# Kernel tuning notes

Hardware: AMD Instinct MI355X
Metric: run time of the kernel (lower is better)

Reference implementation:

```python
import jax, jax.numpy as jnp
import numpy as np

HEADS = 8


def setup_inputs() -> dict:
    key = jax.random.key(0)
    ks = jax.random.split(key, 6)
    B, N, D = 4, 2048, 512
    return {
        "x": jax.random.normal(ks[0], (B, N, D), dtype=jnp.float32),
        "pos": jax.random.uniform(ks[1], (B, N, 3), dtype=jnp.float32),
        "qkv_w": jax.random.normal(ks[2], (3 * D, D), dtype=jnp.float32) * 0.02,
        "qkv_b": jax.random.normal(ks[3], (3 * D,), dtype=jnp.float32) * 0.02,
        "out_w": jax.random.normal(ks[4], (D, D), dtype=jnp.float32) * 0.02,
        "out_b": jax.random.normal(ks[5], (D,), dtype=jnp.float32) * 0.02,
    }


def reference(x, pos, qkv_w, qkv_b, out_w, out_b):
    B, N, D = x.shape
    H = HEADS
    Dh = D // H
    scale = D ** (-0.5)  # NOTE: original uses full dim, not head dim

    # QKV projection -> [3, B, H, N, Dh]
    qkv = (x @ qkv_w.T + qkv_b).reshape(B, N, 3, H, Dh).transpose(2, 0, 3, 1, 4)
    q, k, v = qkv[0], qkv[1], qkv[2]

    # partial 3D RoPE on first 6 head dims (3 axis pairs)
    theta = pos * jnp.pi                    # [B, N, 3]
    sin = jnp.sin(theta)[:, None]           # [B, 1, N, 3] broadcasts over heads
    cos = jnp.cos(theta)[:, None]

    def rotate(t):
        x_rot = t[..., :6]
        x1 = x_rot[..., 0::2]               # [B, H, N, 3]
        x2 = x_rot[..., 1::2]
        return jnp.concatenate(
            [x1 * cos - x2 * sin, x1 * sin + x2 * cos, t[..., 6:]], axis=-1
        )

    q = rotate(q)
    k = rotate(k)

    attn = jax.nn.softmax(jnp.einsum("bhqd,bhkd->bhqk", q, k) * scale, axis=-1)
    out = jnp.einsum("bhqk,bhkd->bhqd", attn, v)          # [B, H, N, Dh]
    out = out.transpose(0, 2, 1, 3).reshape(B, N, D)
    return out @ out_w.T + out_b
```

## Files before the change

kernel.cpp:

```cpp
#include <hip/hip_runtime.h>
#include <stdint.h>

typedef __attribute__((ext_vector_type(4))) float f32x4;
typedef __attribute__((ext_vector_type(16))) float f32x16;
typedef __attribute__((ext_vector_type(8))) short bf16x8;
typedef __attribute__((ext_vector_type(4))) unsigned short u16x4;

__device__ __forceinline__ unsigned short f2bf(float f) {
    unsigned int u = __builtin_bit_cast(unsigned int, f);
    u += 0x7fffu + ((u >> 16) & 1u);
    return (unsigned short)(u >> 16);
}
__device__ __forceinline__ float bf2f(unsigned short s) {
    unsigned int u = ((unsigned int)s) << 16;
    return __builtin_bit_cast(float, u);
}
__device__ __forceinline__ float fexp2(float x) {
#if __has_builtin(__builtin_amdgcn_exp2f)
    return __builtin_amdgcn_exp2f(x);
#else
    return exp2f(x);
#endif
}
__device__ __forceinline__ unsigned int cvt_pk_bf16(float lo, float hi) {
    unsigned int r;
    asm("v_cvt_pk_bf16_f32 %0, %1, %2" : "=v"(r) : "v"(lo), "v"(hi));
    return r;
}

__global__ void k_cvt3(const float* __restrict__ x,
                       const float* __restrict__ w1,
                       const float* __restrict__ w2,
                       unsigned short* __restrict__ out) {
    const int C1 = 1048576;
    const int C2 = 196608;
    int i = blockIdx.x * blockDim.x + threadIdx.x;
    f32x4 v;
    if (i < C1)            v = ((const f32x4*)x)[i];
    else if (i < C1 + C2)  v = ((const f32x4*)w1)[i - C1];
    else                   v = ((const f32x4*)w2)[i - C1 - C2];
    u16x4 o;
    o.x = f2bf(v.x); o.y = f2bf(v.y); o.z = f2bf(v.z); o.w = f2bf(v.w);
    ((u16x4*)out)[i] = o;
}

__global__ __launch_bounds__(256, 3)
void k_gemm_qkv(const unsigned short* __restrict__ A,
                const unsigned short* __restrict__ Bm,
                const float* __restrict__ bias,
                const float* __restrict__ pos,
                unsigned short* __restrict__ Qb,
                unsigned short* __restrict__ Kb,
                unsigned short* __restrict__ VT) {
    const float PI = 3.14159265358979323846f;
    const float QS = 0.04419417382415922f * 1.44269504088896341f;
    const int K = 512, N = 1536;
    __shared__ unsigned short As[3][128 * 32];
    __shared__ unsigned short Bs[3][128 * 32];
    const int tid = threadIdx.x;
    const int lane = tid & 63;
    const int w = tid >> 6;
    const int wr = (w >> 1) * 64, wc = (w & 1) * 64;
    const int g = lane >> 4, fr = lane & 15;

    const int bid = blockIdx.x;
    const int xcd = bid & 7, loc = bid >> 3;
    const int rowb = xcd * 8 + (loc & 7);
    const int colb = loc >> 3;

    f32x4 acc[4][4];
#pragma unroll
    for (int i = 0; i < 4; ++i)
#pragma unroll
        for (int j = 0; j < 4; ++j) acc[i][j] = f32x4{0.f, 0.f, 0.f, 0.f};

    const int srow16 = lane >> 2;
    const int schunk = ((lane & 3) ^ (srow16 & 3)) * 8;
    const int sA = w, sB = w + 4;
    const unsigned short* Aseg0 = A + (size_t)(rowb * 128 + sA * 16 + srow16) * K + schunk;
    const unsigned short* Aseg1 = A + (size_t)(rowb * 128 + sB * 16 + srow16) * K + schunk;
    const unsigned short* Bseg0 = Bm + (size_t)(colb * 128 + sA * 16 + srow16) * K + schunk;
    const unsigned short* Bseg1 = Bm + (size_t)(colb * 128 + sB * 16 + srow16) * K + schunk;

    auto stage = [&](int bsel, int k0) {
        char* la = (char*)&As[bsel][0];
        char* lb = (char*)&Bs[bsel][0];
        __builtin_amdgcn_global_load_lds((const __attribute__((address_space(1))) void*)(Aseg0 + k0),
                                         (__attribute__((address_space(3))) void*)(la + sA * 1024), 16, 0, 0);
        __builtin_amdgcn_global_load_lds((const __attribute__((address_space(1))) void*)(Aseg1 + k0),
                                         (__attribute__((address_space(3))) void*)(la + sB * 1024), 16, 0, 0);
        __builtin_amdgcn_global_load_lds((const __attribute__((address_space(1))) void*)(Bseg0 + k0),
                                         (__attribute__((address_space(3))) void*)(lb + sA * 1024), 16, 0, 0);
        __builtin_amdgcn_global_load_lds((const __attribute__((address_space(1))) void*)(Bseg1 + k0),
                                         (__attribute__((address_space(3))) void*)(lb + sB * 1024), 16, 0, 0);
    };
    auto compute = [&](int bsel) {
        bf16x8 af[4], bfv[4];
        const int rc = (g ^ (fr & 3)) * 8;
#pragma unroll
        for (int mi = 0; mi < 4; ++mi)
            af[mi] = *(const bf16x8*)&As[bsel][(wr + mi * 16 + fr) * 32 + rc];
#pragma unroll
        for (int ni = 0; ni < 4; ++ni)
            bfv[ni] = *(const bf16x8*)&Bs[bsel][(wc + ni * 16 + fr) * 32 + rc];
        __builtin_amdgcn_s_setprio(1);
#pragma unroll
        for (int mi = 0; mi < 4; ++mi)
#pragma unroll
            for (int ni = 0; ni < 4; ++ni)
                acc[mi][ni] = __builtin_amdgcn_mfma_f32_16x16x32_bf16(af[mi], bfv[ni], acc[mi][ni], 0, 0, 0);
        __builtin_amdgcn_s_setprio(0);
    };

    const int nt = K >> 5;
    stage(0, 0);
    stage(1, 32);
    int cur = 0;
#pragma unroll 1
    for (int t = 0; t < nt; ++t) {
        if (t < nt - 1) asm volatile("s_waitcnt vmcnt(4)" ::: "memory");
        else            asm volatile("s_waitcnt vmcnt(0)" ::: "memory");
        __builtin_amdgcn_s_barrier();
        compute(cur);
        if (t + 2 < nt) {
            int nxt = cur + 2; if (nxt >= 3) nxt -= 3;
            stage(nxt, (t + 2) << 5);
        }
        cur = (cur + 1 == 3) ? 0 : cur + 1;
    }

    const int jrot = (fr < 3) ? fr : ((fr < 6) ? fr - 3 : 0);
    const int shbase = lane & 48;
#pragma unroll
    for (int mi = 0; mi < 4; ++mi) {
#pragma unroll
        for (int ni = 0; ni < 4; ++ni) {
            int row = rowb * 128 + wr + mi * 16 + g * 4;
            int col = colb * 128 + wc + ni * 16 + fr;
            float bz = bias[col];
            float v[4];
#pragma unroll
            for (int r = 0; r < 4; ++r) v[r] = acc[mi][ni][r] + bz;
            int b = row >> 11, n = row & 2047;
            if (colb < 8) {
                const int isQ = (colb < 4);
                int qcol = isQ ? col : col - 512;
                int h = qcol >> 6, dh = qcol & 63;
                if (ni == 0) {
#pragma unroll
                    for (int r = 0; r < 4; ++r) {
                        float x1 = __shfl(v[r], shbase + 2 * jrot, 64);
                        float x2 = __shfl(v[r], shbase + 2 * jrot + 1, 64);
                        if (fr < 6) {
                            float th = pos[(row + r) * 3 + jrot] * PI;
                            float sn = __sinf(th), cs = __cosf(th);
                            v[r] = (fr < 3) ? (x1 * cs - x2 * sn) : (x1 * sn + x2 * cs);
                        }
                    }
                }
                float qs = isQ ? QS : 1.f;
                unsigned short* dst = isQ ? Qb : Kb;
                size_t rb = (size_t)(b * 8 + h) * 2048 + n;
#pragma unroll
                for (int r = 0; r < 4; ++r)
                    dst[(rb + r) * 64 + dh] = f2bf(v[r] * qs);
            } else {
                int vcol = col - 1024;
                int h = vcol >> 6, dh = vcol & 63;
                int q2 = (n >> 2) & 3;
                int np = n + (q2 == 1 ? 4 : (q2 == 2 ? -4 : 0));
                u16x4 o;
#pragma unroll
                for (int r = 0; r < 4; ++r) o[r] = f2bf(v[r]);
                *(u16x4*)&VT[((size_t)(b * 8 + h) * 64 + dh) * 2048 + np] = o;
            }
        }
    }
}

__global__ __launch_bounds__(256, 3)
void k_gemm_out(const unsigned short* __restrict__ A,
                const unsigned short* __restrict__ Bm,
                const float* __restrict__ bias,
                float* __restrict__ Cout, int M, int N, int K) {
    __shared__ unsigned short As[3][128 * 32];
    __shared__ unsigned short Bs[3][128 * 32];
    const int tid = threadIdx.x;
    const int lane = tid & 63;
    const int w = tid >> 6;
    const int wr = (w >> 1) * 64, wc = (w & 1) * 64;
    const int g = lane >> 4, fr = lane & 15;

    const int bid = blockIdx.x;
    const int xcd = bid & 7, loc = bid >> 3;
    const int rowb = xcd * 8 + (loc & 7);
    const int colb = loc >> 3;

    f32x4 acc[4][4];
#pragma unroll
    for (int i = 0; i < 4; ++i)
#pragma unroll
        for (int j = 0; j < 4; ++j) acc[i][j] = f32x4{0.f, 0.f, 0.f, 0.f};

    const int srow16 = lane >> 2;
    const int schunk = ((lane & 3) ^ (srow16 & 3)) * 8;
    const int sA = w, sB = w + 4;
    const unsigned short* Aseg0 = A + (size_t)(rowb * 128 + sA * 16 + srow16) * K + schunk;
    const unsigned short* Aseg1 = A + (size_t)(rowb * 128 + sB * 16 + srow16) * K + schunk;
    const unsigned short* Bseg0 = Bm + (size_t)(colb * 128 + sA * 16 + srow16) * K + schunk;
    const unsigned short* Bseg1 = Bm + (size_t)(colb * 128 + sB * 16 + srow16) * K + schunk;

    auto stage = [&](int bsel, int k0) {
        char* la = (char*)&As[bsel][0];
        char* lb = (char*)&Bs[bsel][0];
        __builtin_amdgcn_global_load_lds((const __attribute__((address_space(1))) void*)(Aseg0 + k0),
                                         (__attribute__((address_space(3))) void*)(la + sA * 1024), 16, 0, 0);
        __builtin_amdgcn_global_load_lds((const __attribute__((address_space(1))) void*)(Aseg1 + k0),
                                         (__attribute__((address_space(3))) void*)(la + sB * 1024), 16, 0, 0);
        __builtin_amdgcn_global_load_lds((const __attribute__((address_space(1))) void*)(Bseg0 + k0),
                                         (__attribute__((address_space(3))) void*)(lb + sA * 1024), 16, 0, 0);
        __builtin_amdgcn_global_load_lds((const __attribute__((address_space(1))) void*)(Bseg1 + k0),
                                         (__attribute__((address_space(3))) void*)(lb + sB * 1024), 16, 0, 0);
    };
    auto compute = [&](int bsel) {
        bf16x8 af[4], bfv[4];
        const int rc = (g ^ (fr & 3)) * 8;
#pragma unroll
        for (int mi = 0; mi < 4; ++mi)
            af[mi] = *(const bf16x8*)&As[bsel][(wr + mi * 16 + fr) * 32 + rc];
#pragma unroll
        for (int ni = 0; ni < 4; ++ni)
            bfv[ni] = *(const bf16x8*)&Bs[bsel][(wc + ni * 16 + fr) * 32 + rc];
        __builtin_amdgcn_s_setprio(1);
#pragma unroll
        for (int mi = 0; mi < 4; ++mi)
#pragma unroll
            for (int ni = 0; ni < 4; ++ni)
                acc[mi][ni] = __builtin_amdgcn_mfma_f32_16x16x32_bf16(af[mi], bfv[ni], acc[mi][ni], 0, 0, 0);
        __builtin_amdgcn_s_setprio(0);
    };

    const int nt = K >> 5;
    stage(0, 0);
    stage(1, 32);
    int cur = 0;
#pragma unroll 1
    for (int t = 0; t < nt; ++t) {
        if (t < nt - 1) asm volatile("s_waitcnt vmcnt(4)" ::: "memory");
        else            asm volatile("s_waitcnt vmcnt(0)" ::: "memory");
        __builtin_amdgcn_s_barrier();
        compute(cur);
        if (t + 2 < nt) {
            int nxt = cur + 2; if (nxt >= 3) nxt -= 3;
            stage(nxt, (t + 2) << 5);
        }
        cur = (cur + 1 == 3) ? 0 : cur + 1;
    }

#pragma unroll
    for (int mi = 0; mi < 4; ++mi) {
#pragma unroll
        for (int ni = 0; ni < 4; ++ni) {
            int row = rowb * 128 + wr + mi * 16 + g * 4;
            int col = colb * 128 + wc + ni * 16 + fr;
            float bz = bias[col];
#pragma unroll
            for (int r = 0; r < 4; ++r)
                Cout[(size_t)(row + r) * N + col] = acc[mi][ni][r] + bz;
        }
    }
}

__global__ __launch_bounds__(512, 4)
void k_attn(const unsigned short* __restrict__ Qb,
            const unsigned short* __restrict__ Kb,
            const unsigned short* __restrict__ VT,
            unsigned short* __restrict__ Ob) {
    __shared__ unsigned short smem[2][2][2][4096];
    const int tid = threadIdx.x, lane = tid & 63, w = tid >> 6;
    const int wl = w & 3, half = w >> 2;
    const int l31 = lane & 31, hi = lane >> 5;
    const int bid = blockIdx.x;
    const int bh = (bid & 7) * 4 + ((bid >> 3) >> 4);
    const int qb = (bid >> 3) & 15;
    const int b = bh >> 3, h = bh & 7;
    const int qr0 = qb * 128 + wl * 32;
    const unsigned short* Q = Qb + (size_t)bh * 2048 * 64;
    const unsigned short* K = Kb + (size_t)bh * 2048 * 64;
    const unsigned short* V = VT + (size_t)bh * 64 * 2048;
    const int thalf = half * 16;

    const int srow8 = lane >> 3;
    const int swc = ((lane & 7) ^ srow8) << 3;
    const int sA = wl, sB = wl + 4;

    bf16x8 bq[4];
#pragma unroll
    for (int ds = 0; ds < 4; ++ds)
        bq[ds] = *(const bf16x8*)&Q[(size_t)(qr0 + l31) * 64 + ds * 16 + hi * 8];

    f32x16 oT0, oT1;
#pragma unroll
    for (int i = 0; i < 16; ++i) { oT0[i] = 0.f; oT1[i] = 0.f; }
    float lpart = 0.f;

    auto stage = [&](int bsel, int t) {
        const int kv0 = t * 64;
        const unsigned short* k0 = K + (size_t)(kv0 + sA * 8 + srow8) * 64 + swc;
        const unsigned short* k1 = K + (size_t)(kv0 + sB * 8 + srow8) * 64 + swc;
        const unsigned short* v0 = V + (size_t)(sA * 8 + srow8) * 2048 + kv0 + swc;
        const unsigned short* v1 = V + (size_t)(sB * 8 + srow8) * 2048 + kv0 + swc;
        char* dk = (char*)&smem[half][0][bsel][0];
        char* dv = (char*)&smem[half][1][bsel][0];
        __builtin_amdgcn_global_load_lds((const __attribute__((address_space(1))) void*)k0,
                                         (__attribute__((address_space(3))) void*)(dk + sA * 1024), 16, 0, 0);
        __builtin_amdgcn_global_load_lds((const __attribute__((address_space(1))) void*)k1,
                                         (__attribute__((address_space(3))) void*)(dk + sB * 1024), 16, 0, 0);
        __builtin_amdgcn_global_load_lds((const __attribute__((address_space(1))) void*)v0,
                                         (__attribute__((address_space(3))) void*)(dv + sA * 1024), 16, 0, 0);
        __builtin_amdgcn_global_load_lds((const __attribute__((address_space(1))) void*)v1,
                                         (__attribute__((address_space(3))) void*)(dv + sB * 1024), 16, 0, 0);
    };

    auto pack8 = [&](const float* p) -> bf16x8 {
        union { unsigned int u[4]; bf16x8 v; } c;
        c.u[0] = cvt_pk_bf16(p[0], p[1]);
        c.u[1] = cvt_pk_bf16(p[2], p[3]);
        c.u[2] = cvt_pk_bf16(p[4], p[5]);
        c.u[3] = cvt_pk_bf16(p[6], p[7]);
        return c.v;
    };

    auto compute = [&](int bsel) {
        const unsigned short* KsC = &smem[half][0][bsel][0];
        const unsigned short* VtC = &smem[half][1][bsel][0];
        f32x16 s0, s1;
#pragma unroll
        for (int i = 0; i < 16; ++i) { s0[i] = 0.f; s1[i] = 0.f; }
        __builtin_amdgcn_s_setprio(1);
#pragma unroll
        for (int ds = 0; ds < 4; ++ds) {
            const int c = ((((ds << 1) | hi) ^ (l31 & 7)) << 3);
            bf16x8 ka0 = *(const bf16x8*)&KsC[l31 * 64 + c];
            bf16x8 ka1 = *(const bf16x8*)&KsC[(32 + l31) * 64 + c];
            s0 = __builtin_amdgcn_mfma_f32_32x32x16_bf16(ka0, bq[ds], s0, 0, 0, 0);
            s1 = __builtin_amdgcn_mfma_f32_32x32x16_bf16(ka1, bq[ds], s1, 0, 0, 0);
        }
        __builtin_amdgcn_s_setprio(0);
        float p0[16], p1[16];
        float lsum = 0.f;
#pragma unroll
        for (int r = 0; r < 16; ++r) {
            p0[r] = fexp2(s0[r]);
            p1[r] = fexp2(s1[r]);
            lsum += p0[r] + p1[r];
        }
        lpart += lsum;
        bf16x8 pb0 = pack8(p0);
        bf16x8 pb1 = pack8(p0 + 8);
        bf16x8 pb2 = pack8(p1);
        bf16x8 pb3 = pack8(p1 + 8);
        __builtin_amdgcn_s_setprio(1);
#pragma unroll
        for (int kb = 0; kb < 4; ++kb) {
            const int c = ((((kb << 1) | hi) ^ (l31 & 7)) << 3);
            bf16x8 av0 = *(const bf16x8*)&VtC[l31 * 64 + c];
            bf16x8 av1 = *(const bf16x8*)&VtC[(32 + l31) * 64 + c];
            bf16x8 pbk = (kb == 0) ? pb0 : (kb == 1) ? pb1 : (kb == 2) ? pb2 : pb3;
            oT0 = __builtin_amdgcn_mfma_f32_32x32x16_bf16(av0, pbk, oT0, 0, 0, 0);
            oT1 = __builtin_amdgcn_mfma_f32_32x32x16_bf16(av1, pbk, oT1, 0, 0, 0);
        }
        __builtin_amdgcn_s_setprio(0);
    };

    stage(0, thalf);
    asm volatile("s_waitcnt vmcnt(0)" ::: "memory");
    __builtin_amdgcn_s_barrier();
    int cur = 0;
#pragma unroll 1
    for (int t = 0; t < 16; ++t) {
        if (t < 15) stage(cur ^ 1, thalf + t + 1);
        compute(cur);
        if (t < 15) {
            asm volatile("s_waitcnt vmcnt(0)" ::: "memory");
            __builtin_amdgcn_s_barrier();
        }
        cur ^= 1;
    }

    __syncthreads();
    float* mrg = (float*)&smem[0][0][0][0];
    float* slot = mrg + (size_t)(wl * 64 + lane) * 33;
    if (half) {
#pragma unroll
        for (int i = 0; i < 16; ++i) { slot[i] = oT0[i]; slot[16 + i] = oT1[i]; }
        slot[32] = lpart;
    }
    __syncthreads();
    if (!half) {
#pragma unroll
        for (int i = 0; i < 16; ++i) { oT0[i] += slot[i]; oT1[i] += slot[16 + i]; }
        float lf = lpart + slot[32];
        lf += __shfl_xor(lf, 32, 64);
        float il = 1.f / lf;
        size_t rowbase = (size_t)(b * 2048 + qr0 + l31) * 512 + h * 64;
#pragma unroll
        for (int grp = 0; grp < 4; ++grp) {
            u16x4 o0, o1;
#pragma unroll
            for (int i = 0; i < 4; ++i) {
                o0[i] = f2bf(oT0[grp * 4 + i] * il);
                o1[i] = f2bf(oT1[grp * 4 + i] * il);
            }
            int dv0 = grp * 8 + 4 * hi;
            *(u16x4*)&Ob[rowbase + dv0] = o0;
            *(u16x4*)&Ob[rowbase + 32 + dv0] = o1;
        }
    }
}

extern "C" void kernel_launch(void* const* d_in, const int* in_sizes, int n_in,
                              void* d_out, int out_size, void* d_ws, size_t ws_size,
                              hipStream_t stream) {
    const float* x     = (const float*)d_in[0];
    const float* pos   = (const float*)d_in[1];
    const float* qkv_w = (const float*)d_in[2];
    const float* qkv_b = (const float*)d_in[3];
    const float* out_w = (const float*)d_in[4];
    const float* out_b = (const float*)d_in[5];
    float* out = (float*)d_out;

    unsigned short* Xb   = (unsigned short*)d_ws;
    unsigned short* W1b  = Xb   + (size_t)8192 * 512;
    unsigned short* W2b  = W1b  + (size_t)1536 * 512;
    unsigned short* Qb   = W2b  + (size_t)512 * 512;
    unsigned short* Kb   = Qb   + (size_t)4194304;
    unsigned short* VTb  = Kb   + (size_t)4194304;
    unsigned short* Ob   = VTb  + (size_t)4194304;

    k_cvt3<<<5120, 256, 0, stream>>>(x, qkv_w, out_w, Xb);
    k_gemm_qkv<<<768, 256, 0, stream>>>(Xb, W1b, qkv_b, pos, Qb, Kb, VTb);
    k_attn<<<512, 512, 0, stream>>>(Qb, Kb, VTb, Ob);
    k_gemm_out<<<256, 256, 0, stream>>>(Ob, W2b, out_b, out, 8192, 512, 512);
}
```

Baseline: 85.60 us.

## Process two query sub-tiles per wave in attention to reuse K/V tiles

The attention kernel now gives each wave 64 query rows (two 32-row sub-tiles) instead of 32, doubling the query block per workgroup to 256 and halving the grid to 256 blocks. Each staged K/V tile in LDS is reused for twice as many queries, which halves global-to-LDS traffic and barrier count per query. The PV MFMAs for the first sub-tile are interleaved with the exp work of the second sub-tile so matrix and vector units can overlap. In exchange, register pressure roughly doubles (launch bounds lowered to 2 blocks/SM) and fewer blocks may underfill the 256 CUs.

```diff
diff --git a/kernel.cpp b/kernel.cpp
--- a/kernel.cpp
+++ b/kernel.cpp
@@ -54,7 +54,7 @@
                 unsigned short* __restrict__ VT) {
     const float PI = 3.14159265358979323846f;
     const float QS = 0.04419417382415922f * 1.44269504088896341f;
-    const int K = 512, N = 1536;
+    const int K = 512;
     __shared__ unsigned short As[3][128 * 32];
     __shared__ unsigned short Bs[3][128 * 32];
     const int tid = threadIdx.x;
@@ -271,7 +271,7 @@
     }
 }
 
-__global__ __launch_bounds__(512, 4)
+__global__ __launch_bounds__(512, 2)
 void k_attn(const unsigned short* __restrict__ Qb,
             const unsigned short* __restrict__ Kb,
             const unsigned short* __restrict__ VT,
@@ -281,10 +281,11 @@
     const int wl = w & 3, half = w >> 2;
     const int l31 = lane & 31, hi = lane >> 5;
     const int bid = blockIdx.x;
-    const int bh = (bid & 7) * 4 + ((bid >> 3) >> 4);
-    const int qb = (bid >> 3) & 15;
+    const int loc = bid >> 3;
+    const int bh = (bid & 7) * 4 + (loc >> 3);
+    const int qb = loc & 7;
     const int b = bh >> 3, h = bh & 7;
-    const int qr0 = qb * 128 + wl * 32;
+    const int qr0 = qb * 256 + wl * 64;
     const unsigned short* Q = Qb + (size_t)bh * 2048 * 64;
     const unsigned short* K = Kb + (size_t)bh * 2048 * 64;
     const unsigned short* V = VT + (size_t)bh * 64 * 2048;
@@ -294,15 +295,17 @@
     const int swc = ((lane & 7) ^ srow8) << 3;
     const int sA = wl, sB = wl + 4;
 
-    bf16x8 bq[4];
-#pragma unroll
-    for (int ds = 0; ds < 4; ++ds)
-        bq[ds] = *(const bf16x8*)&Q[(size_t)(qr0 + l31) * 64 + ds * 16 + hi * 8];
-
-    f32x16 oT0, oT1;
-#pragma unroll
-    for (int i = 0; i < 16; ++i) { oT0[i] = 0.f; oT1[i] = 0.f; }
-    float lpart = 0.f;
+    bf16x8 bq0[4], bq1[4];
+#pragma unroll
+    for (int ds = 0; ds < 4; ++ds) {
+        bq0[ds] = *(const bf16x8*)&Q[(size_t)(qr0 + l31) * 64 + ds * 16 + hi * 8];
+        bq1[ds] = *(const bf16x8*)&Q[(size_t)(qr0 + 32 + l31) * 64 + ds * 16 + hi * 8];
+    }
+
+    f32x16 oT00, oT01, oT10, oT11;
+#pragma unroll
+    for (int i = 0; i < 16; ++i) { oT00[i] = 0.f; oT01[i] = 0.f; oT10[i] = 0.f; oT11[i] = 0.f; }
+    float lp0 = 0.f, lp1 = 0.f;
 
     auto stage = [&](int bsel, int t) {
         const int kv0 = t * 64;
@@ -334,41 +337,75 @@
     auto compute = [&](int bsel) {
         const unsigned short* KsC = &smem[half][0][bsel][0];
         const unsigned short* VtC = &smem[half][1][bsel][0];
-        f32x16 s0, s1;
-#pragma unroll
-        for (int i = 0; i < 16; ++i) { s0[i] = 0.f; s1[i] = 0.f; }
-        __builtin_amdgcn_s_setprio(1);
-#pragma unroll
-        for (int ds = 0; ds < 4; ++ds) {
-            const int c = ((((ds << 1) | hi) ^ (l31 & 7)) << 3);
-            bf16x8 ka0 = *(const bf16x8*)&KsC[l31 * 64 + c];
-            bf16x8 ka1 = *(const bf16x8*)&KsC[(32 + l31) * 64 + c];
-            s0 = __builtin_amdgcn_mfma_f32_32x32x16_bf16(ka0, bq[ds], s0, 0, 0, 0);
-            s1 = __builtin_amdgcn_mfma_f32_32x32x16_bf16(ka1, bq[ds], s1, 0, 0, 0);
-        }
-        __builtin_amdgcn_s_setprio(0);
-        float p0[16], p1[16];
-        float lsum = 0.f;
-#pragma unroll
-        for (int r = 0; r < 16; ++r) {
-            p0[r] = fexp2(s0[r]);
-            p1[r] = fexp2(s1[r]);
-            lsum += p0[r] + p1[r];
-        }
-        lpart += lsum;
-        bf16x8 pb0 = pack8(p0);
-        bf16x8 pb1 = pack8(p0 + 8);
-        bf16x8 pb2 = pack8(p1);
-        bf16x8 pb3 = pack8(p1 + 8);
+        bf16x8 pb0[4], pb1[4];
+        {
+            f32x16 s0, s1;
+#pragma unroll
+            for (int i = 0; i < 16; ++i) { s0[i] = 0.f; s1[i] = 0.f; }
+            __builtin_amdgcn_s_setprio(1);
+#pragma unroll
+            for (int ds = 0; ds < 4; ++ds) {
+                const int c = ((((ds << 1) | hi) ^ (l31 & 7)) << 3);
+                bf16x8 ka0 = *(const bf16x8*)&KsC[l31 * 64 + c];
+                bf16x8 ka1 = *(const bf16x8*)&KsC[(32 + l31) * 64 + c];
+                s0 = __builtin_amdgcn_mfma_f32_32x32x16_bf16(ka0, bq0[ds], s0, 0, 0, 0);
+                s1 = __builtin_amdgcn_mfma_f32_32x32x16_bf16(ka1, bq0[ds], s1, 0, 0, 0);
+            }
+            __builtin_amdgcn_s_setprio(0);
+            float p0[16], p1[16], lsum = 0.f;
+#pragma unroll
+            for (int r = 0; r < 16; ++r) {
+                p0[r] = fexp2(s0[r]);
+                p1[r] = fexp2(s1[r]);
+                lsum += p0[r] + p1[r];
+            }
+            lp0 += lsum;
+            pb0[0] = pack8(p0); pb0[1] = pack8(p0 + 8);
+            pb0[2] = pack8(p1); pb0[3] = pack8(p1 + 8);
+        }
+        {
+            f32x16 s0, s1;
+#pragma unroll
+            for (int i = 0; i < 16; ++i) { s0[i] = 0.f; s1[i] = 0.f; }
+            __builtin_amdgcn_s_setprio(1);
+#pragma unroll
+            for (int ds = 0; ds < 4; ++ds) {
+                const int c = ((((ds << 1) | hi) ^ (l31 & 7)) << 3);
+                bf16x8 ka0 = *(const bf16x8*)&KsC[l31 * 64 + c];
+                bf16x8 ka1 = *(const bf16x8*)&KsC[(32 + l31) * 64 + c];
+                s0 = __builtin_amdgcn_mfma_f32_32x32x16_bf16(ka0, bq1[ds], s0, 0, 0, 0);
+                s1 = __builtin_amdgcn_mfma_f32_32x32x16_bf16(ka1, bq1[ds], s1, 0, 0, 0);
+            }
+            __builtin_amdgcn_s_setprio(0);
+            __builtin_amdgcn_s_setprio(1);
+#pragma unroll
+            for (int kb = 0; kb < 4; ++kb) {
+                const int c = ((((kb << 1) | hi) ^ (l31 & 7)) << 3);
+                bf16x8 av0 = *(const bf16x8*)&VtC[l31 * 64 + c];
+                bf16x8 av1 = *(const bf16x8*)&VtC[(32 + l31) * 64 + c];
+                oT00 = __builtin_amdgcn_mfma_f32_32x32x16_bf16(av0, pb0[kb], oT00, 0, 0, 0);
+                oT01 = __builtin_amdgcn_mfma_f32_32x32x16_bf16(av1, pb0[kb], oT01, 0, 0, 0);
+            }
+            __builtin_amdgcn_s_setprio(0);
+            float p0[16], p1[16], lsum = 0.f;
+#pragma unroll
+            for (int r = 0; r < 16; ++r) {
+                p0[r] = fexp2(s0[r]);
+                p1[r] = fexp2(s1[r]);
+                lsum += p0[r] + p1[r];
+            }
+            lp1 += lsum;
+            pb1[0] = pack8(p0); pb1[1] = pack8(p0 + 8);
+            pb1[2] = pack8(p1); pb1[3] = pack8(p1 + 8);
+        }
         __builtin_amdgcn_s_setprio(1);
 #pragma unroll
         for (int kb = 0; kb < 4; ++kb) {
             const int c = ((((kb << 1) | hi) ^ (l31 & 7)) << 3);
             bf16x8 av0 = *(const bf16x8*)&VtC[l31 * 64 + c];
             bf16x8 av1 = *(const bf16x8*)&VtC[(32 + l31) * 64 + c];
-            bf16x8 pbk = (kb == 0) ? pb0 : (kb == 1) ? pb1 : (kb == 2) ? pb2 : pb3;
-            oT0 = __builtin_amdgcn_mfma_f32_32x32x16_bf16(av0, pbk, oT0, 0, 0, 0);
-            oT1 = __builtin_amdgcn_mfma_f32_32x32x16_bf16(av1, pbk, oT1, 0, 0, 0);
+            oT10 = __builtin_amdgcn_mfma_f32_32x32x16_bf16(av0, pb1[kb], oT10, 0, 0, 0);
+            oT11 = __builtin_amdgcn_mfma_f32_32x32x16_bf16(av1, pb1[kb], oT11, 0, 0, 0);
         }
         __builtin_amdgcn_s_setprio(0);
     };
@@ -388,33 +425,37 @@
         cur ^= 1;
     }
 
-    __syncthreads();
     float* mrg = (float*)&smem[0][0][0][0];
     float* slot = mrg + (size_t)(wl * 64 + lane) * 33;
-    if (half) {
-#pragma unroll
-        for (int i = 0; i < 16; ++i) { slot[i] = oT0[i]; slot[16 + i] = oT1[i]; }
-        slot[32] = lpart;
-    }
-    __syncthreads();
-    if (!half) {
-#pragma unroll
-        for (int i = 0; i < 16; ++i) { oT0[i] += slot[i]; oT1[i] += slot[16 + i]; }
-        float lf = lpart + slot[32];
-        lf += __shfl_xor(lf, 32, 64);
-        float il = 1.f / lf;
-        size_t rowbase = (size_t)(b * 2048 + qr0 + l31) * 512 + h * 64;
-#pragma unroll
-        for (int grp = 0; grp < 4; ++grp) {
-            u16x4 o0, o1;
-#pragma unroll
-            for (int i = 0; i < 4; ++i) {
-                o0[i] = f2bf(oT0[grp * 4 + i] * il);
-                o1[i] = f2bf(oT1[grp * 4 + i] * il);
-            }
-            int dv0 = grp * 8 + 4 * hi;
-            *(u16x4*)&Ob[rowbase + dv0] = o0;
-            *(u16x4*)&Ob[rowbase + 32 + dv0] = o1;
+#pragma unroll 1
+    for (int st = 0; st < 2; ++st) {
+        f32x16& a0 = st ? oT10 : oT00;
+        f32x16& a1 = st ? oT11 : oT01;
+        float lp = st ? lp1 : lp0;
+        __syncthreads();
+        if (half) {
+#pragma unroll
+            for (int i = 0; i < 16; ++i) { slot[i] = a0[i]; slot[16 + i] = a1[i]; }
+            slot[32] = lp;
+        }
+        __syncthreads();
+        if (!half) {
+            float lf = lp + slot[32];
+            lf += __shfl_xor(lf, 32, 64);
+            float il = 1.f / lf;
+            size_t rowbase = (size_t)(b * 2048 + qr0 + st * 32 + l31) * 512 + h * 64;
+#pragma unroll
+            for (int grp = 0; grp < 4; ++grp) {
+                u16x4 o0, o1;
+#pragma unroll
+                for (int i = 0; i < 4; ++i) {
+                    o0[i] = f2bf((a0[grp * 4 + i] + slot[grp * 4 + i]) * il);
+                    o1[i] = f2bf((a1[grp * 4 + i] + slot[16 + grp * 4 + i]) * il);
+                }
+                int dv0 = grp * 8 + 4 * hi;
+                *(u16x4*)&Ob[rowbase + dv0] = o0;
+                *(u16x4*)&Ob[rowbase + 32 + dv0] = o1;
+            }
         }
     }
 }
@@ -440,6 +481,6 @@
 
     k_cvt3<<<5120, 256, 0, stream>>>(x, qkv_w, out_w, Xb);
     k_gemm_qkv<<<768, 256, 0, stream>>>(Xb, W1b, qkv_b, pos, Qb, Kb, VTb);
-    k_attn<<<512, 512, 0, stream>>>(Qb, Kb, VTb, Ob);
+    k_attn<<<256, 512, 0, stream>>>(Qb, Kb, VTb, Ob);
     k_gemm_out<<<256, 256, 0, stream>>>(Ob, W2b, out_b, out, 8192, 512, 512);
 }
```

After: 83.54 us (median of 3 runs). 2.4% less time.

## Drop intra-block KV split in attention, use 4 waves over full KV

Applied to the files above, without the earlier changes.

The attention kernel previously ran 8 waves per block, with two halves each processing half of the key/value sequence and merging partial outputs and sums through shared memory. It now runs 4 waves per block that each iterate over the full 32 KV tiles, removing the LDS merge, the extra barriers and half the shared memory. The trade-off is half as many resident waves in total and a longer serial loop per wave, which may reduce latency hiding. An unused constant in the QKV GEMM is also removed.

```diff
diff --git a/kernel.cpp b/kernel.cpp
--- a/kernel.cpp
+++ b/kernel.cpp
@@ -54,7 +54,7 @@
                 unsigned short* __restrict__ VT) {
     const float PI = 3.14159265358979323846f;
     const float QS = 0.04419417382415922f * 1.44269504088896341f;
-    const int K = 512, N = 1536;
+    const int K = 512;
     __shared__ unsigned short As[3][128 * 32];
     __shared__ unsigned short Bs[3][128 * 32];
     const int tid = threadIdx.x;
@@ -271,28 +271,27 @@
     }
 }
 
-__global__ __launch_bounds__(512, 4)
+__global__ __launch_bounds__(256, 4)
 void k_attn(const unsigned short* __restrict__ Qb,
             const unsigned short* __restrict__ Kb,
             const unsigned short* __restrict__ VT,
             unsigned short* __restrict__ Ob) {
-    __shared__ unsigned short smem[2][2][2][4096];
+    __shared__ unsigned short smem[2][2][4096];
     const int tid = threadIdx.x, lane = tid & 63, w = tid >> 6;
-    const int wl = w & 3, half = w >> 2;
     const int l31 = lane & 31, hi = lane >> 5;
     const int bid = blockIdx.x;
-    const int bh = (bid & 7) * 4 + ((bid >> 3) >> 4);
-    const int qb = (bid >> 3) & 15;
+    const int loc = bid >> 3;
+    const int bh = (bid & 7) * 4 + (loc >> 4);
+    const int qb = loc & 15;
     const int b = bh >> 3, h = bh & 7;
-    const int qr0 = qb * 128 + wl * 32;
+    const int qr0 = qb * 128 + w * 32;
     const unsigned short* Q = Qb + (size_t)bh * 2048 * 64;
     const unsigned short* K = Kb + (size_t)bh * 2048 * 64;
     const unsigned short* V = VT + (size_t)bh * 64 * 2048;
-    const int thalf = half * 16;
 
     const int srow8 = lane >> 3;
     const int swc = ((lane & 7) ^ srow8) << 3;
-    const int sA = wl, sB = wl + 4;
+    const int sA = w, sB = w + 4;
 
     bf16x8 bq[4];
 #pragma unroll
@@ -310,8 +309,8 @@
         const unsigned short* k1 = K + (size_t)(kv0 + sB * 8 + srow8) * 64 + swc;
         const unsigned short* v0 = V + (size_t)(sA * 8 + srow8) * 2048 + kv0 + swc;
         const unsigned short* v1 = V + (size_t)(sB * 8 + srow8) * 2048 + kv0 + swc;
-        char* dk = (char*)&smem[half][0][bsel][0];
-        char* dv = (char*)&smem[half][1][bsel][0];
+        char* dk = (char*)&smem[0][bsel][0];
+        char* dv = (char*)&smem[1][bsel][0];
         __builtin_amdgcn_global_load_lds((const __attribute__((address_space(1))) void*)k0,
                                          (__attribute__((address_space(3))) void*)(dk + sA * 1024), 16, 0, 0);
         __builtin_amdgcn_global_load_lds((const __attribute__((address_space(1))) void*)k1,
@@ -332,8 +331,8 @@
     };
 
     auto compute = [&](int bsel) {
-        const unsigned short* KsC = &smem[half][0][bsel][0];
-        const unsigned short* VtC = &smem[half][1][bsel][0];
+        const unsigned short* KsC = &smem[0][bsel][0];
+        const unsigned short* VtC = &smem[1][bsel][0];
         f32x16 s0, s1;
 #pragma unroll
         for (int i = 0; i < 16; ++i) { s0[i] = 0.f; s1[i] = 0.f; }
@@ -373,49 +372,35 @@
         __builtin_amdgcn_s_setprio(0);
     };
 
-    stage(0, thalf);
+    stage(0, 0);
     asm volatile("s_waitcnt vmcnt(0)" ::: "memory");
     __builtin_amdgcn_s_barrier();
     int cur = 0;
 #pragma unroll 1
-    for (int t = 0; t < 16; ++t) {
-        if (t < 15) stage(cur ^ 1, thalf + t + 1);
+    for (int t = 0; t < 32; ++t) {
+        if (t < 31) stage(cur ^ 1, t + 1);
         compute(cur);
-        if (t < 15) {
+        if (t < 31) {
             asm volatile("s_waitcnt vmcnt(0)" ::: "memory");
             __builtin_amdgcn_s_barrier();
         }
         cur ^= 1;
     }
 
-    __syncthreads();
-    float* mrg = (float*)&smem[0][0][0][0];
-    float* slot = mrg + (size_t)(wl * 64 + lane) * 33;
-    if (half) {
-#pragma unroll
-        for (int i = 0; i < 16; ++i) { slot[i] = oT0[i]; slot[16 + i] = oT1[i]; }
-        slot[32] = lpart;
-    }
-    __syncthreads();
-    if (!half) {
-#pragma unroll
-        for (int i = 0; i < 16; ++i) { oT0[i] += slot[i]; oT1[i] += slot[16 + i]; }
-        float lf = lpart + slot[32];
-        lf += __shfl_xor(lf, 32, 64);
-        float il = 1.f / lf;
-        size_t rowbase = (size_t)(b * 2048 + qr0 + l31) * 512 + h * 64;
-#pragma unroll
-        for (int grp = 0; grp < 4; ++grp) {
-            u16x4 o0, o1;
-#pragma unroll
-            for (int i = 0; i < 4; ++i) {
-                o0[i] = f2bf(oT0[grp * 4 + i] * il);
-                o1[i] = f2bf(oT1[grp * 4 + i] * il);
-            }
-            int dv0 = grp * 8 + 4 * hi;
-            *(u16x4*)&Ob[rowbase + dv0] = o0;
-            *(u16x4*)&Ob[rowbase + 32 + dv0] = o1;
-        }
+    float lf = lpart + __shfl_xor(lpart, 32, 64);
+    float il = 1.f / lf;
+    size_t rowbase = (size_t)(b * 2048 + qr0 + l31) * 512 + h * 64;
+#pragma unroll
+    for (int grp = 0; grp < 4; ++grp) {
+        u16x4 o0, o1;
+#pragma unroll
+        for (int i = 0; i < 4; ++i) {
+            o0[i] = f2bf(oT0[grp * 4 + i] * il);
+            o1[i] = f2bf(oT1[grp * 4 + i] * il);
+        }
+        int dv0 = grp * 8 + 4 * hi;
+        *(u16x4*)&Ob[rowbase + dv0] = o0;
+        *(u16x4*)&Ob[rowbase + 32 + dv0] = o1;
     }
 }
 
@@ -440,6 +425,6 @@
 
     k_cvt3<<<5120, 256, 0, stream>>>(x, qkv_w, out_w, Xb);
     k_gemm_qkv<<<768, 256, 0, stream>>>(Xb, W1b, qkv_b, pos, Qb, Kb, VTb);
-    k_attn<<<512, 512, 0, stream>>>(Qb, Kb, VTb, Ob);
+    k_attn<<<512, 256, 0, stream>>>(Qb, Kb, VTb, Ob);
     k_gemm_out<<<256, 256, 0, stream>>>(Ob, W2b, out_b, out, 8192, 512, 512);
 }
```

Measured after the change: 86.83 us. No clear change (+1.4%).
